# Kernel tuning notes

Measured on AMD Instinct MI355X. Metric: run time of the kernel, lower is better.

## Reference

```python
import jax, jax.numpy as jnp
import numpy as np

N, RANK, M = 512, 32, 4096


def setup_inputs() -> dict:
    key = jax.random.key(0)
    k1, k2, k3 = jax.random.split(key, 3)
    # Module init: randn * 5 for W and H (pre-softplus parameters)
    W = jax.random.normal(k1, (N, RANK), dtype=jnp.float32) * 5.0
    H = jax.random.normal(k2, (RANK, M), dtype=jnp.float32) * 5.0
    # tau starts at zeros in the module but becomes nonzero during fit;
    # use randn so the phase-shift path is exercised.
    tau = jax.random.normal(k3, (N, RANK), dtype=jnp.float32)
    return {"W": W, "H": H, "tau": tau}


def reference(W, H, tau):
    Nf = M // 2 + 1
    # fft of real softplus(H); keep only nonneg freqs then rebuild full spectrum
    Hf = jnp.fft.fft(jax.nn.softplus(H), axis=1)[:, :Nf]          # (rank, Nf) complex64
    Hf_rev = jnp.flip(Hf[:, 1:Nf - 1], axis=1)
    Hft = jnp.concatenate([Hf, jnp.conj(Hf_rev)], axis=1)          # (rank, M)
    f = jnp.arange(M, dtype=jnp.float32) / M                       # (M,)
    # omega[N,d,M] = exp(-2*pi*i * tau[N,d] * f[M])
    phase = jnp.einsum('Nd,M->NdM', tau, f)
    omega = jnp.exp(-1j * 2.0 * jnp.pi * phase)                    # (N, rank, M) complex64
    # V[N,M] = sum_d softplus(W)[N,d] * omega[N,d,M] * Hft[d,M]
    V = jnp.einsum('Nd,NdM,dM->NM', jax.nn.softplus(W).astype(omega.dtype), omega, Hft)
    return V
```

## Files before the change

kernel.cpp:

```cpp
#include <hip/hip_runtime.h>
#include <hip/hip_bf16.h>

#define MM 4096
#define NN 512
#define RR 32

__device__ __forceinline__ float softplus_f(float x) {
    return x > 20.0f ? x : log1pf(__expf(x));
}

__global__ __launch_bounds__(1024) void fft_rows_kernel(const float* __restrict__ H,
                                                        float2* __restrict__ hft) {
    __shared__ float2 buf[2][MM];
    const int d   = blockIdx.x;
    const int tid = threadIdx.x;
    const float* Hrow = H + (size_t)d * MM;

    for (int t = tid; t < MM; t += 1024)
        buf[0][t] = make_float2(softplus_f(Hrow[t]), 0.0f);
    __syncthreads();

#pragma unroll
    for (int i = 0; i < 6; ++i) {
        const int   sh    = 2 * i;
        const int   st    = 1 << sh;
        const float inv_n = 1.0f / (float)(MM >> sh);
        const float2* cur = buf[i & 1];
        float2*       nxt = buf[(i & 1) ^ 1];

        const int t = tid;
        const int p = t >> sh;
        const int q = t & (st - 1);

        const float2 a0 = cur[t];
        const float2 a1 = cur[t + 1024];
        const float2 a2 = cur[t + 2048];
        const float2 a3 = cur[t + 3072];

        const float e0x = a0.x + a2.x, e0y = a0.y + a2.y;
        const float e1x = a1.x + a3.x, e1y = a1.y + a3.y;
        const float o0x = a0.x - a2.x, o0y = a0.y - a2.y;
        const float o1x = a1.x - a3.x, o1y = a1.y - a3.y;

        const float2 y0 = make_float2(e0x + e1x, e0y + e1y);
        const float2 y2 = make_float2(e0x - e1x, e0y - e1y);
        const float2 y1 = make_float2(o0x + o1y, o0y - o1x);
        const float2 y3 = make_float2(o0x - o1y, o0y + o1x);

        const float th = (float)p * inv_n;
        const float c1 = __builtin_amdgcn_cosf(th);
        const float s1 = __builtin_amdgcn_sinf(th);
        const float c2 = fmaf(-2.0f * s1, s1, 1.0f);
        const float s2 = 2.0f * s1 * c1;
        const float c3 = c1 * c2 - s1 * s2;
        const float s3 = s1 * c2 + c1 * s2;

        const int base = 4 * t - 3 * q;
        nxt[base]          = y0;
        nxt[base + st]     = make_float2(fmaf(y1.x, c1,  y1.y * s1),
                                         fmaf(y1.y, c1, -y1.x * s1));
        nxt[base + 2*st]   = make_float2(fmaf(y2.x, c2,  y2.y * s2),
                                         fmaf(y2.y, c2, -y2.x * s2));
        nxt[base + 3*st]   = make_float2(fmaf(y3.x, c3,  y3.y * s3),
                                         fmaf(y3.y, c3, -y3.x * s3));
        __syncthreads();
    }

    for (int t = tid; t < MM; t += 1024)
        hft[(size_t)d * MM + t] = buf[0][t];
}

__global__ __launch_bounds__(256) void shiftnmf_real(const float* __restrict__ W,
                                                     const float* __restrict__ tau,
                                                     const float2* __restrict__ hft,
                                                     float* __restrict__ out) {
    __shared__ float spw_s[8][RR];
    __shared__ float tf_s[8][RR];
    __shared__ float cu_s[8][RR];
    __shared__ float su_s[8][RR];
    __shared__ float h2048_s[RR];

    const int tid = threadIdx.x;
    const int mb  = blockIdx.x * 256;
    const int nb  = blockIdx.y * 8;

    {
        const int nl = tid >> 5;
        const int dd = tid & 31;
        const float w = W[(size_t)(nb + nl) * RR + dd];
        const float t = tau[(size_t)(nb + nl) * RR + dd];
        spw_s[nl][dd] = softplus_f(w);
        tf_s[nl][dd]  = t * (1.0f / (float)MM);
        const float fr = t - floorf(t);
        cu_s[nl][dd] =  __builtin_amdgcn_cosf(fr);
        su_s[nl][dd] = -__builtin_amdgcn_sinf(fr);
    }
    if (tid < RR) h2048_s[tid] = hft[(size_t)tid * MM + 2048].x;
    __syncthreads();

    const int g  = tid >> 5;
    const int ml = tid & 31;
    const int n  = nb + g;
    const float m0f = (float)(mb + ml);
    const float2* hcol = hft + mb + ml;

    float accm[8], accp[8];
#pragma unroll
    for (int k = 0; k < 8; ++k) { accm[k] = 0.0f; accp[k] = 0.0f; }

    float2 hc[8], hn[8];
#pragma unroll
    for (int k = 0; k < 8; ++k) hc[k] = hcol[32 * k];

    for (int d = 0; d < RR; ++d) {
        const float2* hnp = hcol + (size_t)((d + 1 < RR) ? d + 1 : d) * MM;
#pragma unroll
        for (int k = 0; k < 8; ++k) hn[k] = hnp[32 * k];

        const float A  = spw_s[g][d];
        const float tf = tf_s[g][d];
        const float ru = cu_s[g][d];
        const float iu = su_s[g][d];

        float r0 = tf * m0f;   r0 -= floorf(r0);
        float dl = tf * 32.0f; dl -= floorf(dl);
        const float c0 = __builtin_amdgcn_cosf(r0);
        const float s0 = __builtin_amdgcn_sinf(r0);
        const float cd = __builtin_amdgcn_cosf(dl);
        const float sd = __builtin_amdgcn_sinf(dl);
        float ca = A * c0, sa = A * s0;
        float cb = ca * cd - sa * sd;
        float sb = sa * cd + ca * sd;
        const float c2 = fmaf(-2.0f * sd, sd, 1.0f);
        const float s2 = 2.0f * sd * cd;

#pragma unroll
        for (int t = 0; t < 4; ++t) {
            const float2 h0 = hc[2 * t];
            const float2 h1 = hc[2 * t + 1];
            const float rz0 = fmaf(ca, h0.x,   sa * h0.y);
            const float iz0 = fmaf(ca, h0.y, -(sa * h0.x));
            accm[2 * t]     += rz0;
            accp[2 * t]      = fmaf(ru, rz0, fmaf(iu, iz0, accp[2 * t]));
            const float rz1 = fmaf(cb, h1.x,   sb * h1.y);
            const float iz1 = fmaf(cb, h1.y, -(sb * h1.x));
            accm[2 * t + 1] += rz1;
            accp[2 * t + 1]  = fmaf(ru, rz1, fmaf(iu, iz1, accp[2 * t + 1]));
            if (t < 3) {
                const float can = fmaf(ca, c2, -(sa * s2));
                const float san = fmaf(sa, c2,  (ca * s2));
                const float cbn = fmaf(cb, c2, -(sb * s2));
                const float sbn = fmaf(sb, c2,  (cb * s2));
                ca = can; sa = san; cb = cbn; sb = sbn;
            }
        }
#pragma unroll
        for (int k = 0; k < 8; ++k) hc[k] = hn[k];
    }

    float* orow = out + (size_t)n * MM;
#pragma unroll
    for (int k = 0; k < 8; ++k) {
        const int m = mb + ml + 32 * k;
        orow[m] = accm[k];
        if (m != 0) orow[MM - m] = accp[k];
    }

    if (blockIdx.x == 0 && ml == 0) {
        float acc = 0.0f;
        for (int d = 0; d < RR; ++d) {
            float r = tf_s[g][d] * 2048.0f;
            r -= floorf(r);
            acc = fmaf(spw_s[g][d] * h2048_s[d], __builtin_amdgcn_cosf(r), acc);
        }
        orow[2048] = acc;
    }
}

__global__ __launch_bounds__(256) void shiftnmf_cplx(const float* __restrict__ W,
                                                     const float* __restrict__ tau,
                                                     const float2* __restrict__ hft,
                                                     float* __restrict__ out) {
    __shared__ float spw_s[16][RR];
    __shared__ float tau_s[16][RR];

    const int tid = threadIdx.x;
    const int mb  = blockIdx.x * 256;
    const int nb  = blockIdx.y * 16;

    for (int idx = tid; idx < 16 * RR; idx += 256) {
        const int nl = idx >> 5;
        const int dd = idx & 31;
        spw_s[nl][dd] = softplus_f(W[(size_t)(nb + nl) * RR + dd]);
        tau_s[nl][dd] = tau[(size_t)(nb + nl) * RR + dd] * (1.0f / (float)MM);
    }
    __syncthreads();

    const int g  = tid >> 5;
    const int ml = tid & 31;
    const int n0 = g * 2;
    const float m0f = (float)(mb + ml);
    const float2* hcol = hft + mb + ml;

    float accR[2][8], accI[2][8];
#pragma unroll
    for (int j = 0; j < 2; ++j)
#pragma unroll
        for (int k = 0; k < 8; ++k) { accR[j][k] = 0.0f; accI[j][k] = 0.0f; }

    float2 hc[8], hn[8];
#pragma unroll
    for (int k = 0; k < 8; ++k) hc[k] = hcol[32 * k];

    for (int d = 0; d < RR; ++d) {
        const float2* hnp = hcol + (size_t)((d + 1 < RR) ? d + 1 : d) * MM;
#pragma unroll
        for (int k = 0; k < 8; ++k) hn[k] = hnp[32 * k];

#pragma unroll
        for (int j = 0; j < 2; ++j) {
            const float A  = spw_s[n0 + j][d];
            const float tf = tau_s[n0 + j][d];
            float r0 = tf * m0f;  r0 -= floorf(r0);
            float dl = tf * 32.0f; dl -= floorf(dl);
            const float c0 = __builtin_amdgcn_cosf(r0);
            const float s0 = __builtin_amdgcn_sinf(r0);
            const float cd = __builtin_amdgcn_cosf(dl);
            const float sd = __builtin_amdgcn_sinf(dl);
            float ca = A * c0, sa = A * s0;
            float cb = ca * cd - sa * sd;
            float sb = sa * cd + ca * sd;
            const float c2 = fmaf(-2.0f * sd, sd, 1.0f);
            const float s2 = 2.0f * sd * cd;

#pragma unroll
            for (int t4 = 0; t4 < 4; ++t4) {
                const float2 h0 = hc[2 * t4];
                const float2 h1 = hc[2 * t4 + 1];
                accR[j][2*t4]   = fmaf(ca, h0.x, fmaf(sa, h0.y, accR[j][2*t4]));
                accR[j][2*t4+1] = fmaf(cb, h1.x, fmaf(sb, h1.y, accR[j][2*t4+1]));
                accI[j][2*t4]   = fmaf(ca, h0.y, fmaf(-sa, h0.x, accI[j][2*t4]));
                accI[j][2*t4+1] = fmaf(cb, h1.y, fmaf(-sb, h1.x, accI[j][2*t4+1]));
                if (t4 < 3) {
                    const float can = fmaf(ca, c2, -(sa * s2));
                    const float san = fmaf(sa, c2,  (ca * s2));
                    const float cbn = fmaf(cb, c2, -(sb * s2));
                    const float sbn = fmaf(sb, c2,  (cb * s2));
                    ca = can; sa = san; cb = cbn; sb = sbn;
                }
            }
        }
#pragma unroll
        for (int k = 0; k < 8; ++k) hc[k] = hn[k];
    }

#pragma unroll
    for (int j = 0; j < 2; ++j) {
        float2* orow = (float2*)out + (size_t)(nb + n0 + j) * MM + mb + ml;
#pragma unroll
        for (int k = 0; k < 8; ++k)
            orow[32 * k] = make_float2(accR[j][k], accI[j][k]);
    }
}

extern "C" void kernel_launch(void* const* d_in, const int* in_sizes, int n_in,
                              void* d_out, int out_size, void* d_ws, size_t ws_size,
                              hipStream_t stream) {
    const float* W   = (const float*)d_in[0];
    const float* H   = (const float*)d_in[1];
    const float* tau = (const float*)d_in[2];

    const size_t hft_bytes = (size_t)RR * MM * sizeof(float2);
    if (ws_size < hft_bytes) return;
    float2* hft = (float2*)d_ws;

    fft_rows_kernel<<<RR, 1024, 0, stream>>>(H, hft);

    if (out_size >= 2 * NN * MM) {
        dim3 grid(MM / 256, NN / 16);
        shiftnmf_cplx<<<grid, 256, 0, stream>>>(W, tau, hft, (float*)d_out);
    } else {
        dim3 grid(2048 / 256, NN / 8);
        shiftnmf_real<<<grid, 256, 0, stream>>>(W, tau, hft, (float*)d_out);
    }
}
```

Measured before the change: 30.94 us.

## Stage H spectrum tiles in double-buffered LDS and halve per-block columns

The real-output kernel now loads 8-row chunks of the transformed H spectrum into a double-buffered shared-memory tile, prefetching the next chunk into registers while computing on the current one. Each block now covers 128 columns instead of 256, doubling the grid, and each thread keeps 4 accumulator pairs instead of 8. This replaces per-thread global gathers with shared-memory reads, aiming for better latency hiding and occupancy. The cost is an extra barrier per chunk and recomputing the per-d twiddle setup over twice as many blocks.

```diff
diff --git a/kernel.cpp b/kernel.cpp
--- a/kernel.cpp
+++ b/kernel.cpp
@@ -74,14 +74,15 @@
                                                      const float* __restrict__ tau,
                                                      const float2* __restrict__ hft,
                                                      float* __restrict__ out) {
-    __shared__ float spw_s[8][RR];
-    __shared__ float tf_s[8][RR];
-    __shared__ float cu_s[8][RR];
-    __shared__ float su_s[8][RR];
-    __shared__ float h2048_s[RR];
+    __shared__ float2 htile[2][8][128];
+    __shared__ float  spw_s[8][RR];
+    __shared__ float  tf_s[8][RR];
+    __shared__ float  cu_s[8][RR];
+    __shared__ float  su_s[8][RR];
+    __shared__ float  h2048_s[RR];
 
     const int tid = threadIdx.x;
-    const int mb  = blockIdx.x * 256;
+    const int mb  = blockIdx.x * 128;
     const int nb  = blockIdx.y * 8;
 
     {
@@ -96,74 +97,114 @@
         su_s[nl][dd] = -__builtin_amdgcn_sinf(fr);
     }
     if (tid < RR) h2048_s[tid] = hft[(size_t)tid * MM + 2048].x;
+
+    {
+#pragma unroll
+        for (int jj = 0; jj < 4; ++jj) {
+            const int idx = tid + 256 * jj;
+            const int r   = idx >> 7;
+            const int cl  = idx & 127;
+            htile[0][r][cl] = hft[(size_t)r * MM + mb + cl];
+        }
+    }
     __syncthreads();
 
     const int g  = tid >> 5;
     const int ml = tid & 31;
     const int n  = nb + g;
     const float m0f = (float)(mb + ml);
-    const float2* hcol = hft + mb + ml;
-
-    float accm[8], accp[8];
-#pragma unroll
-    for (int k = 0; k < 8; ++k) { accm[k] = 0.0f; accp[k] = 0.0f; }
-
-    float2 hc[8], hn[8];
-#pragma unroll
-    for (int k = 0; k < 8; ++k) hc[k] = hcol[32 * k];
-
-    for (int d = 0; d < RR; ++d) {
-        const float2* hnp = hcol + (size_t)((d + 1 < RR) ? d + 1 : d) * MM;
-#pragma unroll
-        for (int k = 0; k < 8; ++k) hn[k] = hnp[32 * k];
-
-        const float A  = spw_s[g][d];
-        const float tf = tf_s[g][d];
-        const float ru = cu_s[g][d];
-        const float iu = su_s[g][d];
-
-        float r0 = tf * m0f;   r0 -= floorf(r0);
-        float dl = tf * 32.0f; dl -= floorf(dl);
-        const float c0 = __builtin_amdgcn_cosf(r0);
-        const float s0 = __builtin_amdgcn_sinf(r0);
-        const float cd = __builtin_amdgcn_cosf(dl);
-        const float sd = __builtin_amdgcn_sinf(dl);
-        float ca = A * c0, sa = A * s0;
-        float cb = ca * cd - sa * sd;
-        float sb = sa * cd + ca * sd;
-        const float c2 = fmaf(-2.0f * sd, sd, 1.0f);
-        const float s2 = 2.0f * sd * cd;
-
-#pragma unroll
-        for (int t = 0; t < 4; ++t) {
-            const float2 h0 = hc[2 * t];
-            const float2 h1 = hc[2 * t + 1];
-            const float rz0 = fmaf(ca, h0.x,   sa * h0.y);
-            const float iz0 = fmaf(ca, h0.y, -(sa * h0.x));
-            accm[2 * t]     += rz0;
-            accp[2 * t]      = fmaf(ru, rz0, fmaf(iu, iz0, accp[2 * t]));
-            const float rz1 = fmaf(cb, h1.x,   sb * h1.y);
-            const float iz1 = fmaf(cb, h1.y, -(sb * h1.x));
-            accm[2 * t + 1] += rz1;
-            accp[2 * t + 1]  = fmaf(ru, rz1, fmaf(iu, iz1, accp[2 * t + 1]));
-            if (t < 3) {
+
+    float accm[4], accp[4];
+#pragma unroll
+    for (int j = 0; j < 4; ++j) { accm[j] = 0.0f; accp[j] = 0.0f; }
+
+    for (int c = 0; c < 4; ++c) {
+        float2 nx0, nx1, nx2, nx3;
+        if (c < 3) {
+            const float2* src = hft + (size_t)(8 * (c + 1)) * MM + mb;
+            const int i0 = tid, i1 = tid + 256, i2 = tid + 512, i3 = tid + 768;
+            nx0 = src[(size_t)(i0 >> 7) * MM + (i0 & 127)];
+            nx1 = src[(size_t)(i1 >> 7) * MM + (i1 & 127)];
+            nx2 = src[(size_t)(i2 >> 7) * MM + (i2 & 127)];
+            nx3 = src[(size_t)(i3 >> 7) * MM + (i3 & 127)];
+        }
+
+        const int cb_idx = c & 1;
+#pragma unroll
+        for (int dl = 0; dl < 8; ++dl) {
+            const int d = 8 * c + dl;
+            const float A  = spw_s[g][d];
+            const float tf = tf_s[g][d];
+            const float ru = cu_s[g][d];
+            const float iu = su_s[g][d];
+
+            float r0 = tf * m0f;   r0 -= floorf(r0);
+            float dlr = tf * 32.0f; dlr -= floorf(dlr);
+            const float c0 = __builtin_amdgcn_cosf(r0);
+            const float s0 = __builtin_amdgcn_sinf(r0);
+            const float cd = __builtin_amdgcn_cosf(dlr);
+            const float sd = __builtin_amdgcn_sinf(dlr);
+            float ca = A * c0, sa = A * s0;
+            float cb = ca * cd - sa * sd;
+            float sb = sa * cd + ca * sd;
+            const float c2 = fmaf(-2.0f * sd, sd, 1.0f);
+            const float s2 = 2.0f * sd * cd;
+
+            const float2 h0 = htile[cb_idx][dl][ml];
+            const float2 h1 = htile[cb_idx][dl][ml + 32];
+            const float2 h2 = htile[cb_idx][dl][ml + 64];
+            const float2 h3 = htile[cb_idx][dl][ml + 96];
+
+            {
+                const float rz = fmaf(ca, h0.x,   sa * h0.y);
+                const float iz = fmaf(ca, h0.y, -(sa * h0.x));
+                accm[0] += rz;
+                accp[0]  = fmaf(ru, rz, fmaf(iu, iz, accp[0]));
+            }
+            {
+                const float rz = fmaf(cb, h1.x,   sb * h1.y);
+                const float iz = fmaf(cb, h1.y, -(sb * h1.x));
+                accm[1] += rz;
+                accp[1]  = fmaf(ru, rz, fmaf(iu, iz, accp[1]));
+            }
+            {
                 const float can = fmaf(ca, c2, -(sa * s2));
                 const float san = fmaf(sa, c2,  (ca * s2));
                 const float cbn = fmaf(cb, c2, -(sb * s2));
                 const float sbn = fmaf(sb, c2,  (cb * s2));
                 ca = can; sa = san; cb = cbn; sb = sbn;
             }
-        }
-#pragma unroll
-        for (int k = 0; k < 8; ++k) hc[k] = hn[k];
+            {
+                const float rz = fmaf(ca, h2.x,   sa * h2.y);
+                const float iz = fmaf(ca, h2.y, -(sa * h2.x));
+                accm[2] += rz;
+                accp[2]  = fmaf(ru, rz, fmaf(iu, iz, accp[2]));
+            }
+            {
+                const float rz = fmaf(cb, h3.x,   sb * h3.y);
+                const float iz = fmaf(cb, h3.y, -(sb * h3.x));
+                accm[3] += rz;
+                accp[3]  = fmaf(ru, rz, fmaf(iu, iz, accp[3]));
+            }
+        }
+
+        if (c < 3) {
+            float2 (*dst)[128] = htile[(c + 1) & 1];
+            const int i0 = tid, i1 = tid + 256, i2 = tid + 512, i3 = tid + 768;
+            dst[i0 >> 7][i0 & 127] = nx0;
+            dst[i1 >> 7][i1 & 127] = nx1;
+            dst[i2 >> 7][i2 & 127] = nx2;
+            dst[i3 >> 7][i3 & 127] = nx3;
+        }
+        __syncthreads();
     }
 
     float* orow = out + (size_t)n * MM;
 #pragma unroll
-    for (int k = 0; k < 8; ++k) {
-        const int m = mb + ml + 32 * k;
-        orow[m] = accm[k];
-        if (m != 0) orow[MM - m] = accp[k];
+    for (int j = 0; j < 4; ++j) {
+        const int m = mb + ml + 32 * j;
+        orow[m] = accm[j];
+        if (m != 0) orow[MM - m] = accp[j];
     }
 
     if (blockIdx.x == 0 && ml == 0) {
@@ -280,7 +321,7 @@
         dim3 grid(MM / 256, NN / 16);
         shiftnmf_cplx<<<grid, 256, 0, stream>>>(W, tau, hft, (float*)d_out);
     } else {
-        dim3 grid(2048 / 256, NN / 8);
+        dim3 grid(2048 / 128, NN / 8);
         shiftnmf_real<<<grid, 256, 0, stream>>>(W, tau, hft, (float*)d_out);
     }
 }
```

New measurement: 32.12 us. 3.8% more time.

## Replace single-block row FFT with two-pass 64x64 wave-shuffle FFT

Applied to the files above, without the earlier changes.

The 4096-point FFT per rank row, previously run by one 1024-thread block per row (only 32 blocks) with shared-memory radix-4 stages, is replaced by a four-step 64x64 decomposition. Two kernels each launch 512 blocks, and each wavefront does a 64-point FFT using cross-lane shuffles, with a twiddle multiply and a transpose through a global scratch buffer. This gives far more parallelism on the GPU at the cost of an extra kernel launch, an intermediate global round trip and twice the workspace. The rewrite of the inner accumulation loop in the main kernel only rescopes temporaries.

```diff
diff --git a/kernel.cpp b/kernel.cpp
--- a/kernel.cpp
+++ b/kernel.cpp
@@ -9,65 +9,65 @@
     return x > 20.0f ? x : log1pf(__expf(x));
 }
 
-__global__ __launch_bounds__(1024) void fft_rows_kernel(const float* __restrict__ H,
-                                                        float2* __restrict__ hft) {
-    __shared__ float2 buf[2][MM];
-    const int d   = blockIdx.x;
-    const int tid = threadIdx.x;
-    const float* Hrow = H + (size_t)d * MM;
-
-    for (int t = tid; t < MM; t += 1024)
-        buf[0][t] = make_float2(softplus_f(Hrow[t]), 0.0f);
-    __syncthreads();
-
-#pragma unroll
-    for (int i = 0; i < 6; ++i) {
-        const int   sh    = 2 * i;
-        const int   st    = 1 << sh;
-        const float inv_n = 1.0f / (float)(MM >> sh);
-        const float2* cur = buf[i & 1];
-        float2*       nxt = buf[(i & 1) ^ 1];
-
-        const int t = tid;
-        const int p = t >> sh;
-        const int q = t & (st - 1);
-
-        const float2 a0 = cur[t];
-        const float2 a1 = cur[t + 1024];
-        const float2 a2 = cur[t + 2048];
-        const float2 a3 = cur[t + 3072];
-
-        const float e0x = a0.x + a2.x, e0y = a0.y + a2.y;
-        const float e1x = a1.x + a3.x, e1y = a1.y + a3.y;
-        const float o0x = a0.x - a2.x, o0y = a0.y - a2.y;
-        const float o1x = a1.x - a3.x, o1y = a1.y - a3.y;
-
-        const float2 y0 = make_float2(e0x + e1x, e0y + e1y);
-        const float2 y2 = make_float2(e0x - e1x, e0y - e1y);
-        const float2 y1 = make_float2(o0x + o1y, o0y - o1x);
-        const float2 y3 = make_float2(o0x - o1y, o0y + o1x);
-
-        const float th = (float)p * inv_n;
-        const float c1 = __builtin_amdgcn_cosf(th);
-        const float s1 = __builtin_amdgcn_sinf(th);
-        const float c2 = fmaf(-2.0f * s1, s1, 1.0f);
-        const float s2 = 2.0f * s1 * c1;
-        const float c3 = c1 * c2 - s1 * s2;
-        const float s3 = s1 * c2 + c1 * s2;
-
-        const int base = 4 * t - 3 * q;
-        nxt[base]          = y0;
-        nxt[base + st]     = make_float2(fmaf(y1.x, c1,  y1.y * s1),
-                                         fmaf(y1.y, c1, -y1.x * s1));
-        nxt[base + 2*st]   = make_float2(fmaf(y2.x, c2,  y2.y * s2),
-                                         fmaf(y2.y, c2, -y2.x * s2));
-        nxt[base + 3*st]   = make_float2(fmaf(y3.x, c3,  y3.y * s3),
-                                         fmaf(y3.y, c3, -y3.x * s3));
-        __syncthreads();
-    }
-
-    for (int t = tid; t < MM; t += 1024)
-        hft[(size_t)d * MM + t] = buf[0][t];
+__device__ __forceinline__ int bitrev6(int l) {
+    return ((l & 1) << 5) | ((l & 2) << 3) | ((l & 4) << 1) |
+           ((l & 8) >> 1) | ((l & 16) >> 3) | ((l & 32) >> 5);
+}
+
+__device__ __forceinline__ void wave_fft64(float& xr, float& xi) {
+#pragma unroll
+    for (int s = 32; s >= 1; s >>= 1) {
+        const float pr = __shfl_xor(xr, s, 64);
+        const float pi = __shfl_xor(xi, s, 64);
+        const int   lane = threadIdx.x & 63;
+        const bool  hi = (lane & s) != 0;
+        const float ur = xr + pr, ui = xi + pi;
+        const float vr = pr - xr, vi = pi - xi;
+        const int   j  = lane & (s - 1);
+        const float rev = (float)j * (1.0f / (float)(2 * s));
+        const float ct = __builtin_amdgcn_cosf(rev);
+        const float st = __builtin_amdgcn_sinf(rev);
+        const float wr = fmaf(vr, ct,   vi * st);
+        const float wi = fmaf(vi, ct, -(vr * st));
+        xr = hi ? wr : ur;
+        xi = hi ? wi : ui;
+    }
+}
+
+__global__ __launch_bounds__(256) void fft64_step1(const float* __restrict__ H,
+                                                   float2* __restrict__ zbuf) {
+    const int wave = (blockIdx.x * 256 + threadIdx.x) >> 6;
+    const int lane = threadIdx.x & 63;
+    const int d    = wave >> 6;
+    const int n1   = wave & 63;
+
+    float xr = softplus_f(H[(size_t)d * MM + n1 + 64 * lane]);
+    float xi = 0.0f;
+    wave_fft64(xr, xi);
+
+    const int k2 = bitrev6(lane);
+    const float rev = (float)(n1 * k2) * (1.0f / 4096.0f);
+    const float ct = __builtin_amdgcn_cosf(rev);
+    const float st = __builtin_amdgcn_sinf(rev);
+    const float zr = fmaf(xr, ct,   xi * st);
+    const float zi = fmaf(xi, ct, -(xr * st));
+
+    zbuf[(size_t)d * MM + k2 * 64 + n1] = make_float2(zr, zi);
+}
+
+__global__ __launch_bounds__(256) void fft64_step2(const float2* __restrict__ zbuf,
+                                                   float2* __restrict__ hft) {
+    const int wave = (blockIdx.x * 256 + threadIdx.x) >> 6;
+    const int lane = threadIdx.x & 63;
+    const int d    = wave >> 6;
+    const int k2   = wave & 63;
+
+    const float2 z = zbuf[(size_t)d * MM + k2 * 64 + lane];
+    float xr = z.x, xi = z.y;
+    wave_fft64(xr, xi);
+
+    const int k1 = bitrev6(lane);
+    hft[(size_t)d * MM + k2 + 64 * k1] = make_float2(xr, xi);
 }
 
 __global__ __launch_bounds__(256) void shiftnmf_real(const float* __restrict__ W,
@@ -138,14 +138,18 @@
         for (int t = 0; t < 4; ++t) {
             const float2 h0 = hc[2 * t];
             const float2 h1 = hc[2 * t + 1];
-            const float rz0 = fmaf(ca, h0.x,   sa * h0.y);
-            const float iz0 = fmaf(ca, h0.y, -(sa * h0.x));
-            accm[2 * t]     += rz0;
-            accp[2 * t]      = fmaf(ru, rz0, fmaf(iu, iz0, accp[2 * t]));
-            const float rz1 = fmaf(cb, h1.x,   sb * h1.y);
-            const float iz1 = fmaf(cb, h1.y, -(sb * h1.x));
-            accm[2 * t + 1] += rz1;
-            accp[2 * t + 1]  = fmaf(ru, rz1, fmaf(iu, iz1, accp[2 * t + 1]));
+            {
+                const float rz = fmaf(ca, h0.x,   sa * h0.y);
+                const float iz = fmaf(ca, h0.y, -(sa * h0.x));
+                accm[2 * t]     += rz;
+                accp[2 * t]      = fmaf(ru, rz, fmaf(iu, iz, accp[2 * t]));
+            }
+            {
+                const float rz = fmaf(cb, h1.x,   sb * h1.y);
+                const float iz = fmaf(cb, h1.y, -(sb * h1.x));
+                accm[2 * t + 1] += rz;
+                accp[2 * t + 1]  = fmaf(ru, rz, fmaf(iu, iz, accp[2 * t + 1]));
+            }
             if (t < 3) {
                 const float can = fmaf(ca, c2, -(sa * s2));
                 const float san = fmaf(sa, c2,  (ca * s2));
@@ -271,10 +275,12 @@
     const float* tau = (const float*)d_in[2];
 
     const size_t hft_bytes = (size_t)RR * MM * sizeof(float2);
-    if (ws_size < hft_bytes) return;
-    float2* hft = (float2*)d_ws;
-
-    fft_rows_kernel<<<RR, 1024, 0, stream>>>(H, hft);
+    if (ws_size < 2 * hft_bytes) return;
+    float2* zbuf = (float2*)d_ws;
+    float2* hft  = zbuf + (size_t)RR * MM;
+
+    fft64_step1<<<512, 256, 0, stream>>>(H, zbuf);
+    fft64_step2<<<512, 256, 0, stream>>>(zbuf, hft);
 
     if (out_size >= 2 * NN * MM) {
         dim3 grid(MM / 256, NN / 16);
```

After: 30.72 us. Within noise of the previous version (-0.7%).
